# Optimization experiments

Hardware: AMD Instinct MI355X
Metric: run time of the kernel (lower is better)

Reference implementation:

```python
import jax, jax.numpy as jnp
import numpy as np

N = 100000      # nodes
E = 1600000     # edges (avg degree 16)
D_IN = 128
D_H = 128
D_OUT = 64


def setup_inputs() -> dict:
    key = jax.random.key(0)
    ks = jax.random.split(key, 8)
    x = jax.random.normal(ks[0], (N, D_IN), dtype=jnp.float32)
    edge_index = jax.random.randint(ks[1], (2, E), 0, N, dtype=jnp.int64)
    # PyG GraphConv params: lin_rel (with bias) applied to aggregated messages,
    # lin_root (no bias) applied to self features. Kaiming-ish init scale.
    s1 = 1.0 / np.sqrt(D_IN)
    s2 = 1.0 / np.sqrt(D_H)
    W_rel1 = jax.random.uniform(ks[2], (D_H, D_IN), jnp.float32, -s1, s1)
    b_rel1 = jax.random.uniform(ks[3], (D_H,), jnp.float32, -s1, s1)
    W_root1 = jax.random.uniform(ks[4], (D_H, D_IN), jnp.float32, -s1, s1)
    W_rel2 = jax.random.uniform(ks[5], (D_OUT, D_H), jnp.float32, -s2, s2)
    b_rel2 = jax.random.uniform(ks[6], (D_OUT,), jnp.float32, -s2, s2)
    W_root2 = jax.random.uniform(ks[7], (D_OUT, D_H), jnp.float32, -s2, s2)
    return {
        "x": x, "edge_index": edge_index,
        "W_rel1": W_rel1, "b_rel1": b_rel1, "W_root1": W_root1,
        "W_rel2": W_rel2, "b_rel2": b_rel2, "W_root2": W_root2,
    }


def _graph_conv(x, src, dst, W_rel, b_rel, W_root):
    # sum-aggregate neighbor features x[src] into destination nodes,
    # then out = lin_rel(agg) + lin_root(x)  (PyG GraphConv, aggr='add')
    agg = jax.ops.segment_sum(x[src], dst, num_segments=x.shape[0])  # [N, d_in]
    return agg @ W_rel.T + b_rel + x @ W_root.T                      # [N, d_out]


def reference(x, edge_index, W_rel1, b_rel1, W_root1, W_rel2, b_rel2, W_root2):
    src, dst = edge_index[0], edge_index[1]
    h = jax.nn.relu(_graph_conv(x, src, dst, W_rel1, b_rel1, W_root1))  # [N, D_H]
    out = _graph_conv(h, src, dst, W_rel2, b_rel2, W_root2)             # [N, D_OUT]
    # reshape(-1, 1, output_dim) + cat over relations (relations == 1)
    return out.reshape(-1, 1, D_OUT)
```

## Files before the change

### kernel.cpp

```cpp
#include <hip/hip_runtime.h>
#include <hip/hip_bf16.h>


#define BM 128
#define BK 32
#define NPASS 8

typedef unsigned short ushort_t;

__device__ __forceinline__ ushort_t f2bf(float f) {
    unsigned int u = __float_as_uint(f);
    unsigned int r = (u + 0x7fff + ((u >> 16) & 1)) >> 16;
    return (ushort_t)r;
}

__device__ __forceinline__ void bf2x(unsigned int v, float& lo, float& hi) {
    lo = __uint_as_float(v << 16);
    hi = __uint_as_float(v & 0xffff0000u);
}


__global__ __launch_bounds__(256) void hist_kernel(const int* __restrict__ dst,
                                                   int* __restrict__ deg, int E, int N) {
    const int pass = blockIdx.x & (NPASS - 1);
    const int chunk = blockIdx.x >> 3;
    const int rangeSize = (N + NPASS - 1) / NPASS;
    const int lo = pass * rangeSize;
    const int hi = (lo + rangeSize < N) ? lo + rangeSize : N;
    const int base = chunk * 1024 + threadIdx.x * 4;
    if (base + 3 < E) {
        const int4 d4 = *(const int4*)(dst + base);
        if (d4.x >= lo && d4.x < hi) atomicAdd(&deg[d4.x], 1);
        if (d4.y >= lo && d4.y < hi) atomicAdd(&deg[d4.y], 1);
        if (d4.z >= lo && d4.z < hi) atomicAdd(&deg[d4.z], 1);
        if (d4.w >= lo && d4.w < hi) atomicAdd(&deg[d4.w], 1);
    } else {
        for (int i = 0; i < 4; ++i) {
            int e = base + i;
            if (e < E) {
                int d = dst[e];
                if (d >= lo && d < hi) atomicAdd(&deg[d], 1);
            }
        }
    }
}

__global__ __launch_bounds__(256) void scan1_kernel(const int* __restrict__ deg,
                                                    int* __restrict__ bsum, int N) {
    int t = threadIdx.x;
    int base = blockIdx.x * 1024 + t * 4;
    int s = 0;
    if (base + 3 < N) {
        int4 v = *(const int4*)(deg + base);
        s = v.x + v.y + v.z + v.w;
    } else {
#pragma unroll
        for (int i = 0; i < 4; ++i)
            if (base + i < N) s += deg[base + i];
    }
#pragma unroll
    for (int d = 32; d > 0; d >>= 1) s += __shfl_down(s, d);
    __shared__ int wsum[4];
    int lane = t & 63, w = t >> 6;
    if (lane == 0) wsum[w] = s;
    __syncthreads();
    if (t == 0) bsum[blockIdx.x] = wsum[0] + wsum[1] + wsum[2] + wsum[3];
}

__global__ __launch_bounds__(256) void scan2_kernel(const int* __restrict__ bsum,
                                                    int* __restrict__ boff,
                                                    int* __restrict__ offN, int B) {
    __shared__ int s[256];
    int t = threadIdx.x;
    int v = (t < B) ? bsum[t] : 0;
    s[t] = v;
    __syncthreads();
    for (int d = 1; d < 256; d <<= 1) {
        int u = (t >= d) ? s[t - d] : 0;
        __syncthreads();
        s[t] += u;
        __syncthreads();
    }
    if (t < B) boff[t] = s[t] - v;
    if (t == B - 1) *offN = s[t];
}

__global__ __launch_bounds__(256) void scan3_kernel(const int* __restrict__ deg,
                                                    const int* __restrict__ boff,
                                                    int* __restrict__ off,
                                                    int* __restrict__ cursor, int N) {
    int t = threadIdx.x;
    int base = blockIdx.x * 1024 + t * 4;
    int d0 = 0, d1 = 0, d2 = 0, d3 = 0;
    if (base + 3 < N) {
        int4 v = *(const int4*)(deg + base);
        d0 = v.x; d1 = v.y; d2 = v.z; d3 = v.w;
    } else {
        if (base + 0 < N) d0 = deg[base + 0];
        if (base + 1 < N) d1 = deg[base + 1];
        if (base + 2 < N) d2 = deg[base + 2];
    }
    int s = d0 + d1 + d2 + d3;
    int lane = t & 63, w = t >> 6;
    int incl = s;
#pragma unroll
    for (int d = 1; d < 64; d <<= 1) {
        int u = __shfl_up(incl, d);
        if (lane >= d) incl += u;
    }
    __shared__ int wsum[4];
    if (lane == 63) wsum[w] = incl;
    __syncthreads();
    int wpre = 0;
#pragma unroll
    for (int i = 0; i < 3; ++i)
        if (i < w) wpre += wsum[i];
    int excl = incl - s + wpre + boff[blockIdx.x];
    int e0 = excl, e1 = e0 + d0, e2 = e1 + d1, e3 = e2 + d2;
    if (base + 3 < N) {
        *(int4*)(off + base) = make_int4(e0, e1, e2, e3);
        *(int4*)(cursor + base) = make_int4(e0, e1, e2, e3);
    } else {
        if (base + 0 < N) { off[base + 0] = e0; cursor[base + 0] = e0; }
        if (base + 1 < N) { off[base + 1] = e1; cursor[base + 1] = e1; }
        if (base + 2 < N) { off[base + 2] = e2; cursor[base + 2] = e2; }
    }
}

__global__ __launch_bounds__(256) void fill_kernel(const int* __restrict__ src,
                                                   const int* __restrict__ dst,
                                                   int* __restrict__ cursor,
                                                   int* __restrict__ csr, int E, int N) {
    const int pass = blockIdx.x & (NPASS - 1);
    const int chunk = blockIdx.x >> 3;
    const int rangeSize = (N + NPASS - 1) / NPASS;
    const int lo = pass * rangeSize;
    const int hi = (lo + rangeSize < N) ? lo + rangeSize : N;
    const int base = chunk * 1024 + threadIdx.x * 4;
    if (base + 3 < E) {
        const int4 s4 = *(const int4*)(src + base);
        const int4 d4 = *(const int4*)(dst + base);
        if (d4.x >= lo && d4.x < hi) csr[atomicAdd(&cursor[d4.x], 1)] = s4.x;
        if (d4.y >= lo && d4.y < hi) csr[atomicAdd(&cursor[d4.y], 1)] = s4.y;
        if (d4.z >= lo && d4.z < hi) csr[atomicAdd(&cursor[d4.z], 1)] = s4.z;
        if (d4.w >= lo && d4.w < hi) csr[atomicAdd(&cursor[d4.w], 1)] = s4.w;
    } else {
        for (int i = 0; i < 4; ++i) {
            int e = base + i;
            if (e < E) {
                int d = dst[e];
                if (d >= lo && d < hi) csr[atomicAdd(&cursor[d], 1)] = src[e];
            }
        }
    }
}


template <int BN, int EPI, int OB>
__global__ __launch_bounds__(256, 4)
void gemm_k(const float* __restrict__ X, const float* __restrict__ W,
            const float* __restrict__ AGG, const float* __restrict__ bias,
            void* __restrict__ OUTv, int Nrows) {
    __shared__ float xs[BK][BM + 4];
    __shared__ float wsh[BK][BN + 4];

    const int tid = threadIdx.x;
    const int tc = tid & 15;
    const int tr = tid >> 4;
    const int rowBase = blockIdx.x * BM;
    constexpr int CG = BN / 64;

    float acc[8][4 * CG];
#pragma unroll
    for (int i = 0; i < 8; ++i)
#pragma unroll
        for (int j = 0; j < 4 * CG; ++j) acc[i][j] = 0.f;

    const int srow = tid >> 3;
    const int skq = (tid & 7) * 4;

    for (int kc = 0; kc < 128; kc += BK) {
#pragma unroll
        for (int i = 0; i < 4; ++i) {
            int r = srow + i * 32;
            int g = rowBase + r;
            g = g < Nrows ? g : Nrows - 1;
            const float4 v = *(const float4*)(X + (size_t)g * 128 + kc + skq);
            xs[skq + 0][r] = v.x;
            xs[skq + 1][r] = v.y;
            xs[skq + 2][r] = v.z;
            xs[skq + 3][r] = v.w;
        }
#pragma unroll
        for (int i = 0; i < BN / 32; ++i) {
            int j = srow + i * 32;
            const float4 v = *(const float4*)(W + (size_t)j * 128 + kc + skq);
            wsh[skq + 0][j] = v.x;
            wsh[skq + 1][j] = v.y;
            wsh[skq + 2][j] = v.z;
            wsh[skq + 3][j] = v.w;
        }
        __syncthreads();
#pragma unroll
        for (int k = 0; k < BK; ++k) {
            const float4 xa = *(const float4*)&xs[k][tr * 8];
            const float4 xb = *(const float4*)&xs[k][tr * 8 + 4];
            float xr[8] = {xa.x, xa.y, xa.z, xa.w, xb.x, xb.y, xb.z, xb.w};
            float wv[4 * CG];
            const float4 wa = *(const float4*)&wsh[k][tc * 4];
            wv[0] = wa.x; wv[1] = wa.y; wv[2] = wa.z; wv[3] = wa.w;
            if (CG == 2) {
                const float4 wb = *(const float4*)&wsh[k][64 + tc * 4];
                wv[4] = wb.x; wv[5] = wb.y; wv[6] = wb.z; wv[7] = wb.w;
            }
#pragma unroll
            for (int i = 0; i < 8; ++i)
#pragma unroll
                for (int j = 0; j < 4 * CG; ++j) acc[i][j] += xr[i] * wv[j];
        }
        __syncthreads();
    }

#pragma unroll
    for (int i = 0; i < 8; ++i) {
        int g = rowBase + tr * 8 + i;
        if (g >= Nrows) continue;
#pragma unroll
        for (int cg = 0; cg < CG; ++cg) {
            int c = cg * 64 + tc * 4;
            float4 r;
            r.x = acc[i][cg * 4 + 0];
            r.y = acc[i][cg * 4 + 1];
            r.z = acc[i][cg * 4 + 2];
            r.w = acc[i][cg * 4 + 3];
            if (EPI != 0) {
                const float4 a = *(const float4*)(AGG + (size_t)g * BN + c);
                const float4 bb = *(const float4*)(bias + c);
                r.x += a.x + bb.x;
                r.y += a.y + bb.y;
                r.z += a.z + bb.z;
                r.w += a.w + bb.w;
                if (EPI == 1) {
                    r.x = r.x > 0.f ? r.x : 0.f;
                    r.y = r.y > 0.f ? r.y : 0.f;
                    r.z = r.z > 0.f ? r.z : 0.f;
                    r.w = r.w > 0.f ? r.w : 0.f;
                }
            }
            if (OB) {
                ushort_t* OUT = (ushort_t*)OUTv;
                ushort4 o;
                o.x = f2bf(r.x); o.y = f2bf(r.y); o.z = f2bf(r.z); o.w = f2bf(r.w);
                *(ushort4*)(OUT + (size_t)g * BN + c) = o;
            } else {
                float* OUT = (float*)OUTv;
                *(float4*)(OUT + (size_t)g * BN + c) = r;
            }
        }
    }
}


template <int D>
__global__ __launch_bounds__(256)
void agg_k(const ushort_t* __restrict__ F, const int* __restrict__ csr,
           const int* __restrict__ off, float* __restrict__ OUT, int N) {
    constexpr int LPN = (D == 128) ? 64 : 32;
    constexpr int NPB = 256 / LPN;
    int n = blockIdx.x * NPB + (threadIdx.x / LPN);
    if (n >= N) return;
    int lane = threadIdx.x & (LPN - 1);
    int b = off[n], e = off[n + 1];
    const size_t col = (size_t)lane * 2;
    float a0 = 0.f, a1 = 0.f;
    int i = b;
    for (; i + 4 <= e; i += 4) {
        int s0 = csr[i], s1 = csr[i + 1], s2 = csr[i + 2], s3 = csr[i + 3];
        unsigned int v0 = *(const unsigned int*)(F + (size_t)s0 * D + col);
        unsigned int v1 = *(const unsigned int*)(F + (size_t)s1 * D + col);
        unsigned int v2 = *(const unsigned int*)(F + (size_t)s2 * D + col);
        unsigned int v3 = *(const unsigned int*)(F + (size_t)s3 * D + col);
        float l0, h0, l1, h1, l2, h2, l3, h3;
        bf2x(v0, l0, h0); bf2x(v1, l1, h1); bf2x(v2, l2, h2); bf2x(v3, l3, h3);
        a0 += (l0 + l1) + (l2 + l3);
        a1 += (h0 + h1) + (h2 + h3);
    }
    for (; i < e; ++i) {
        unsigned int v = *(const unsigned int*)(F + (size_t)csr[i] * D + col);
        float l, h;
        bf2x(v, l, h);
        a0 += l; a1 += h;
    }
    float2 r; r.x = a0; r.y = a1;
    *(float2*)(OUT + (size_t)n * D + col) = r;
}

extern "C" void kernel_launch(void* const* d_in, const int* in_sizes, int n_in,
                              void* d_out, int out_size, void* d_ws, size_t ws_size,
                              hipStream_t stream) {
    const float* x   = (const float*)d_in[0];
    const int*   ei  = (const int*)d_in[1];
    const float* Wr1 = (const float*)d_in[2];
    const float* br1 = (const float*)d_in[3];
    const float* Wo1 = (const float*)d_in[4];
    const float* Wr2 = (const float*)d_in[5];
    const float* br2 = (const float*)d_in[6];
    const float* Wo2 = (const float*)d_in[7];
    float* out = (float*)d_out;

    const int N = in_sizes[0] / 128;
    const int E = in_sizes[1] / 2;

    const int* srcv = ei;
    const int* dstv = ei + E;

    float*    h    = (float*)d_ws;
    float*    agg1 = h + (size_t)N * 128;
    float*    agg2 = agg1 + (size_t)N * 128;
    ushort_t* qb   = (ushort_t*)(agg2 + (size_t)N * 64);
    int*      deg  = (int*)(qb + (size_t)N * 128);
    int*      off  = deg + N;
    int*      cur  = off + N + 8;
    int*      csr  = cur + N;
    int*      bsum = csr + E;
    int*      boff = bsum + 256;

    const int gemmBlocks = (N + BM - 1) / BM;
    const int agg128Blocks = (N + 3) / 4;
    const int agg64Blocks = (N + 7) / 8;
    const int B = (N + 1023) / 1024;
    const int edgePassBlocks = ((E + 1023) / 1024) * NPASS;

    hipMemsetAsync(deg, 0, (size_t)N * sizeof(int), stream);
    hist_kernel<<<edgePassBlocks, 256, 0, stream>>>(dstv, deg, E, N);
    scan1_kernel<<<B, 256, 0, stream>>>(deg, bsum, N);
    scan2_kernel<<<1, 256, 0, stream>>>(bsum, boff, off + N, B);
    scan3_kernel<<<B, 256, 0, stream>>>(deg, boff, off, cur, N);
    fill_kernel<<<edgePassBlocks, 256, 0, stream>>>(srcv, dstv, cur, csr, E, N);

    gemm_k<128, 0, 1><<<gemmBlocks, 256, 0, stream>>>(x, Wr1, nullptr, nullptr, qb, N);
    agg_k<128><<<agg128Blocks, 256, 0, stream>>>(qb, csr, off, agg1, N);
    gemm_k<128, 1, 0><<<gemmBlocks, 256, 0, stream>>>(x, Wo1, agg1, br1, h, N);

    gemm_k<64, 0, 1><<<gemmBlocks, 256, 0, stream>>>(h, Wr2, nullptr, nullptr, qb , N);
    agg_k<64><<<agg64Blocks, 256, 0, stream>>>(qb , csr, off, agg2, N);
    gemm_k<64, 2, 0><<<gemmBlocks, 256, 0, stream>>>(h, Wo2, agg2, br2, out, N);
}
```

Before: 518.9 us.

## Store aggregation outputs in bf16 and widen per-lane gather loads

The aggregation kernels now write bf16 instead of fp32, and the epilogue GEMMs read the bf16 aggregate and convert it back. This halves the intermediate write and read traffic. Each lane now gathers 4 bf16 values (8 bytes) per neighbor with half as many lanes per node, which cuts the number of load instructions. The GEMM launch bound drops from 4 to 2 blocks per SM, loosening register limits at the cost of occupancy. Rounding the aggregate to bf16 adds extra precision loss.

```diff
diff --git a/kernel.cpp b/kernel.cpp
--- a/kernel.cpp
+++ b/kernel.cpp
@@ -12,6 +12,10 @@
     unsigned int u = __float_as_uint(f);
     unsigned int r = (u + 0x7fff + ((u >> 16) & 1)) >> 16;
     return (ushort_t)r;
+}
+
+__device__ __forceinline__ float bf2f(ushort_t v) {
+    return __uint_as_float(((unsigned int)v) << 16);
 }
 
 __device__ __forceinline__ void bf2x(unsigned int v, float& lo, float& hi) {
@@ -156,10 +160,10 @@
 }
 
 
-template <int BN, int EPI, int OB>
-__global__ __launch_bounds__(256, 4)
+template <int BN, int EPI, int OB, int AB>
+__global__ __launch_bounds__(256, 2)
 void gemm_k(const float* __restrict__ X, const float* __restrict__ W,
-            const float* __restrict__ AGG, const float* __restrict__ bias,
+            const void* __restrict__ AGGv, const float* __restrict__ bias,
             void* __restrict__ OUTv, int Nrows) {
     __shared__ float xs[BK][BM + 4];
     __shared__ float wsh[BK][BN + 4];
@@ -234,12 +238,20 @@
             r.z = acc[i][cg * 4 + 2];
             r.w = acc[i][cg * 4 + 3];
             if (EPI != 0) {
-                const float4 a = *(const float4*)(AGG + (size_t)g * BN + c);
+                float ax, ay, az, aw;
+                if (AB) {
+                    const ushort_t* A = (const ushort_t*)AGGv;
+                    ushort4 a4 = *(const ushort4*)(A + (size_t)g * BN + c);
+                    ax = bf2f(a4.x); ay = bf2f(a4.y); az = bf2f(a4.z); aw = bf2f(a4.w);
+                } else {
+                    const float4 a = *(const float4*)((const float*)AGGv + (size_t)g * BN + c);
+                    ax = a.x; ay = a.y; az = a.z; aw = a.w;
+                }
                 const float4 bb = *(const float4*)(bias + c);
-                r.x += a.x + bb.x;
-                r.y += a.y + bb.y;
-                r.z += a.z + bb.z;
-                r.w += a.w + bb.w;
+                r.x += ax + bb.x;
+                r.y += ay + bb.y;
+                r.z += az + bb.z;
+                r.w += aw + bb.w;
                 if (EPI == 1) {
                     r.x = r.x > 0.f ? r.x : 0.f;
                     r.y = r.y > 0.f ? r.y : 0.f;
@@ -261,38 +273,51 @@
 }
 
 
-template <int D>
+template <int D, int OB>
 __global__ __launch_bounds__(256)
 void agg_k(const ushort_t* __restrict__ F, const int* __restrict__ csr,
-           const int* __restrict__ off, float* __restrict__ OUT, int N) {
-    constexpr int LPN = (D == 128) ? 64 : 32;
+           const int* __restrict__ off, void* __restrict__ OUTv, int N) {
+    constexpr int LPN = (D == 128) ? 32 : 16;
     constexpr int NPB = 256 / LPN;
     int n = blockIdx.x * NPB + (threadIdx.x / LPN);
     if (n >= N) return;
     int lane = threadIdx.x & (LPN - 1);
     int b = off[n], e = off[n + 1];
-    const size_t col = (size_t)lane * 2;
-    float a0 = 0.f, a1 = 0.f;
+    const size_t col = (size_t)lane * 4;
+    float a0 = 0.f, a1 = 0.f, a2 = 0.f, a3 = 0.f;
     int i = b;
     for (; i + 4 <= e; i += 4) {
         int s0 = csr[i], s1 = csr[i + 1], s2 = csr[i + 2], s3 = csr[i + 3];
-        unsigned int v0 = *(const unsigned int*)(F + (size_t)s0 * D + col);
-        unsigned int v1 = *(const unsigned int*)(F + (size_t)s1 * D + col);
-        unsigned int v2 = *(const unsigned int*)(F + (size_t)s2 * D + col);
-        unsigned int v3 = *(const unsigned int*)(F + (size_t)s3 * D + col);
-        float l0, h0, l1, h1, l2, h2, l3, h3;
-        bf2x(v0, l0, h0); bf2x(v1, l1, h1); bf2x(v2, l2, h2); bf2x(v3, l3, h3);
-        a0 += (l0 + l1) + (l2 + l3);
-        a1 += (h0 + h1) + (h2 + h3);
+        uint2 v0 = *(const uint2*)(F + (size_t)s0 * D + col);
+        uint2 v1 = *(const uint2*)(F + (size_t)s1 * D + col);
+        uint2 v2 = *(const uint2*)(F + (size_t)s2 * D + col);
+        uint2 v3 = *(const uint2*)(F + (size_t)s3 * D + col);
+        float l, h;
+        bf2x(v0.x, l, h); a0 += l; a1 += h;
+        bf2x(v0.y, l, h); a2 += l; a3 += h;
+        bf2x(v1.x, l, h); a0 += l; a1 += h;
+        bf2x(v1.y, l, h); a2 += l; a3 += h;
+        bf2x(v2.x, l, h); a0 += l; a1 += h;
+        bf2x(v2.y, l, h); a2 += l; a3 += h;
+        bf2x(v3.x, l, h); a0 += l; a1 += h;
+        bf2x(v3.y, l, h); a2 += l; a3 += h;
     }
     for (; i < e; ++i) {
-        unsigned int v = *(const unsigned int*)(F + (size_t)csr[i] * D + col);
+        uint2 v = *(const uint2*)(F + (size_t)csr[i] * D + col);
         float l, h;
-        bf2x(v, l, h);
-        a0 += l; a1 += h;
-    }
-    float2 r; r.x = a0; r.y = a1;
-    *(float2*)(OUT + (size_t)n * D + col) = r;
+        bf2x(v.x, l, h); a0 += l; a1 += h;
+        bf2x(v.y, l, h); a2 += l; a3 += h;
+    }
+    if (OB) {
+        ushort_t* OUT = (ushort_t*)OUTv;
+        ushort4 o;
+        o.x = f2bf(a0); o.y = f2bf(a1); o.z = f2bf(a2); o.w = f2bf(a3);
+        *(ushort4*)(OUT + (size_t)n * D + col) = o;
+    } else {
+        float* OUT = (float*)OUTv;
+        float4 r; r.x = a0; r.y = a1; r.z = a2; r.w = a3;
+        *(float4*)(OUT + (size_t)n * D + col) = r;
+    }
 }
 
 extern "C" void kernel_launch(void* const* d_in, const int* in_sizes, int n_in,
@@ -315,10 +340,10 @@
     const int* dstv = ei + E;
 
     float*    h    = (float*)d_ws;
-    float*    agg1 = h + (size_t)N * 128;
-    float*    agg2 = agg1 + (size_t)N * 128;
-    ushort_t* qb   = (ushort_t*)(agg2 + (size_t)N * 64);
-    int*      deg  = (int*)(qb + (size_t)N * 128);
+    ushort_t* qb   = (ushort_t*)(h + (size_t)N * 128);
+    ushort_t* a1b  = qb + (size_t)N * 128;
+    ushort_t* a2b  = a1b + (size_t)N * 128;
+    int*      deg  = (int*)(a2b + (size_t)N * 64);
     int*      off  = deg + N;
     int*      cur  = off + N + 8;
     int*      csr  = cur + N;
@@ -326,8 +351,8 @@
     int*      boff = bsum + 256;
 
     const int gemmBlocks = (N + BM - 1) / BM;
-    const int agg128Blocks = (N + 3) / 4;
-    const int agg64Blocks = (N + 7) / 8;
+    const int agg128Blocks = (N + 7) / 8;
+    const int agg64Blocks = (N + 15) / 16;
     const int B = (N + 1023) / 1024;
     const int edgePassBlocks = ((E + 1023) / 1024) * NPASS;
 
@@ -338,11 +363,11 @@
     scan3_kernel<<<B, 256, 0, stream>>>(deg, boff, off, cur, N);
     fill_kernel<<<edgePassBlocks, 256, 0, stream>>>(srcv, dstv, cur, csr, E, N);
 
-    gemm_k<128, 0, 1><<<gemmBlocks, 256, 0, stream>>>(x, Wr1, nullptr, nullptr, qb, N);
-    agg_k<128><<<agg128Blocks, 256, 0, stream>>>(qb, csr, off, agg1, N);
-    gemm_k<128, 1, 0><<<gemmBlocks, 256, 0, stream>>>(x, Wo1, agg1, br1, h, N);
-
-    gemm_k<64, 0, 1><<<gemmBlocks, 256, 0, stream>>>(h, Wr2, nullptr, nullptr, qb , N);
-    agg_k<64><<<agg64Blocks, 256, 0, stream>>>(qb , csr, off, agg2, N);
-    gemm_k<64, 2, 0><<<gemmBlocks, 256, 0, stream>>>(h, Wo2, agg2, br2, out, N);
-}
+    gemm_k<128, 0, 1, 0><<<gemmBlocks, 256, 0, stream>>>(x, Wr1, nullptr, nullptr, qb, N);
+    agg_k<128, 1><<<agg128Blocks, 256, 0, stream>>>(qb, csr, off, a1b, N);
+    gemm_k<128, 1, 0, 1><<<gemmBlocks, 256, 0, stream>>>(x, Wo1, a1b, br1, h, N);
+
+    gemm_k<64, 0, 1, 0><<<gemmBlocks, 256, 0, stream>>>(h, Wr2, nullptr, nullptr, qb , N);
+    agg_k<64, 1><<<agg64Blocks, 256, 0, stream>>>(qb , csr, off, a2b, N);
+    gemm_k<64, 2, 0, 1><<<gemmBlocks, 256, 0, stream>>>(h, Wo2, a2b, br2, out, N);
+}
```

Result: faster. 493.5 us (-4.9%).
